# Kernel tuning notes

Hardware: AMD Instinct MI355X
Metric: run time of the kernel (lower is better)

The kernel has to match this reference:

```python
import jax, jax.numpy as jnp
import numpy as np

N_NODES = 50000
N_EDGES = 800000
N_GRAPHS = 64
IN_DIM = 128
HID = 64
HEADS = 4
LAT = 32
BN_EPS = 1e-5


def setup_inputs() -> dict:
    key = jax.random.key(0)
    ks = jax.random.split(key, 16)
    x = jax.random.normal(ks[0], (N_NODES, IN_DIM), jnp.float32)
    edge_index = jax.random.randint(ks[1], (2, N_EDGES), 0, N_NODES, dtype=jnp.int64)
    batch = jnp.sort(jax.random.randint(ks[2], (N_NODES,), 0, N_GRAPHS, dtype=jnp.int64))

    def lin(k, fan_in, shape):
        return (jax.random.normal(k, shape, jnp.float32) / np.sqrt(fan_in)).astype(jnp.float32)

    d = {"x": x, "edge_index": edge_index, "batch": batch}
    dims = [IN_DIM, HID, HID]
    i = 3
    for l, din in enumerate(dims):
        d[f"Wl{l}"] = lin(ks[i], din, (din, HEADS * HID)); i += 1
        d[f"Wr{l}"] = lin(ks[i], din, (din, HEADS * HID)); i += 1
        d[f"att{l}"] = lin(ks[i], HID, (HEADS, HID)); i += 1
        d[f"b{l}"] = jnp.zeros((HID,), jnp.float32)
    d["bn_gamma"] = jnp.ones((HID,), jnp.float32)
    d["bn_beta"] = jnp.zeros((HID,), jnp.float32)
    d["fc_W"] = lin(ks[i], HID, (LAT, HID)); i += 1
    d["fc_b"] = jnp.zeros((LAT,), jnp.float32)
    return d


def _gatv2_conv(x, Wl, Wr, att, b, src, dst):
    # PyG GATv2Conv, concat=False: mean over heads. src -> dst message flow.
    n = x.shape[0]
    H, D = att.shape
    xl = (x @ Wl).reshape(n, H, D)   # source-side transform
    xr = (x @ Wr).reshape(n, H, D)   # target-side transform
    e = jax.nn.leaky_relu(xl[src] + xr[dst], 0.2)        # [E, H, D]
    logits = jnp.einsum('ehd,hd->eh', e, att)            # [E, H]
    # segment softmax over incoming edges of each dst node
    m = jax.ops.segment_max(logits, dst, num_segments=n)
    p = jnp.exp(logits - m[dst])
    denom = jax.ops.segment_sum(p, dst, num_segments=n)
    alpha = p / (denom[dst] + 1e-16)                     # [E, H]
    out = jax.ops.segment_sum(alpha[..., None] * xl[src], dst, num_segments=n)  # [N, H, D]
    return out.mean(axis=1) + b


def reference(x, edge_index, batch, Wl0, Wr0, att0, b0, Wl1, Wr1, att1, b1,
              Wl2, Wr2, att2, b2, bn_gamma, bn_beta, fc_W, fc_b):
    src, dst = edge_index[0], edge_index[1]
    h = x
    for (Wl, Wr, att, b) in ((Wl0, Wr0, att0, b0), (Wl1, Wr1, att1, b1), (Wl2, Wr2, att2, b2)):
        h = _gatv2_conv(h, Wl, Wr, att, b, src, dst)
        h = jax.nn.leaky_relu(h, 0.1)
        # dropout omitted (deterministic reference / eval semantics)
    pooled = jax.ops.segment_sum(h, batch, num_segments=N_GRAPHS)  # [G, HID]
    mean = pooled.mean(axis=0)
    var = pooled.var(axis=0)  # biased variance, matches BN training normalization
    y = (pooled - mean) / jnp.sqrt(var + BN_EPS) * bn_gamma + bn_beta
    return y @ fc_W.T + fc_b
```

## Files before the change

kernel.cpp:

```cpp
#include <hip/hip_runtime.h>
#include <hip/hip_bf16.h>
#include <math.h>

#define N_NODES 50000
#define N_EDGES 800000
#define N_GRAPHS 64
#define IN_DIM 128
#define HID 64
#define HEADS 4
#define LAT 32
#define SCAN_BLOCKS ((N_NODES + 255) / 256)
#define ES_CAP 960000

typedef __attribute__((ext_vector_type(8))) short bf16x8;
typedef __attribute__((ext_vector_type(4))) float floatx4;
typedef __attribute__((ext_vector_type(2))) float f32x2;

__device__ inline unsigned short f2bf(float f) {
    unsigned u = __float_as_uint(f);
    return (unsigned short)((u + 0x7fffu + ((u >> 16) & 1u)) >> 16);
}

__device__ inline f32x2 bfpair(unsigned u) {
    f32x2 r;
    r.x = __uint_as_float(u << 16);
    r.y = __uint_as_float(u & 0xffff0000u);
    return r;
}

__device__ inline float rowsum16(float x) {
    x += __int_as_float(__builtin_amdgcn_mov_dpp(__float_as_int(x), 0x128, 0xf, 0xf, false));
    x += __int_as_float(__builtin_amdgcn_mov_dpp(__float_as_int(x), 0x124, 0xf, 0xf, false));
    x += __int_as_float(__builtin_amdgcn_mov_dpp(__float_as_int(x), 0x122, 0xf, 0xf, false));
    x += __int_as_float(__builtin_amdgcn_mov_dpp(__float_as_int(x), 0x121, 0xf, 0xf, false));
    return x;
}

__global__ __launch_bounds__(256) void prep_kernel(
    const float* __restrict__ x, unsigned* __restrict__ xbf,
    const float* __restrict__ Wl0, const float* __restrict__ Wr0,
    const float* __restrict__ Wl1, const float* __restrict__ Wr1,
    const float* __restrict__ Wl2, const float* __restrict__ Wr2,
    unsigned short* __restrict__ B0, unsigned short* __restrict__ B1,
    unsigned short* __restrict__ B2,
    int* __restrict__ cnt, float* __restrict__ pooled, int* __restrict__ done,
    uint4* __restrict__ es4) {
    int b = blockIdx.x, t = threadIdx.x;
    if (b < 3072) {
        for (int i = b * 256 + t; i < N_NODES * IN_DIM / 2; i += 3072 * 256) {
            float2 v = reinterpret_cast<const float2*>(x)[i];
            xbf[i] = (unsigned)f2bf(v.x) | ((unsigned)f2bf(v.y) << 16);
        }
    } else if (b < 3584) {
        int idx = (b - 3072) * 256 + t;
        const float *Wl, *Wr;
        unsigned short* B;
        int KC, local;
        if (idx < 65536)      { Wl = Wl0; Wr = Wr0; B = B0; KC = 4; local = idx; }
        else if (idx < 98304) { Wl = Wl1; Wr = Wr1; B = B1; KC = 2; local = idx - 65536; }
        else                  { Wl = Wl2; Wr = Wr2; B = B2; KC = 2; local = idx - 98304; }
        int j = local & 7;
        int lane = (local >> 3) & 63;
        int rem = local >> 9;
        int kc = rem % KC;
        int tile = rem / KC;
        int k = kc * 32 + (lane >> 4) * 8 + j;
        int tt = tile & 15;
        int n = (tt >> 1) * 32 + 2 * (lane & 15) + (tt & 1);
        const float* W = (tile < 16) ? Wl : Wr;
        B[local] = f2bf(W[k * 256 + n]);
    } else if (b < 3840) {
        int idx = (b - 3584) * 256 + t;
        if (idx < N_NODES) cnt[idx] = 0;
        if (idx < N_GRAPHS * HID) pooled[idx] = 0.f;
        if (idx == 0) *done = 0;
    } else {
        int idx = (b - 3840) * 256 + t;
        for (int i = idx; i < ES_CAP / 4; i += 65536)
            es4[i] = uint4{0, 0, 0, 0};
    }
}

__global__ __launch_bounds__(256) void deg_kernel(const int* __restrict__ dsts,
                                                  int* __restrict__ cnt, int E) {
    int e = blockIdx.x * 256 + threadIdx.x;
    if (e < E) atomicAdd(&cnt[dsts[e]], 1);
}

__global__ __launch_bounds__(256) void scan_kernel(const int* __restrict__ cnt,
                                                   int* __restrict__ offs,
                                                   int* __restrict__ sc,
                                                   int* __restrict__ agg) {
    __shared__ int buf[256];
    int b = blockIdx.x, t = threadIdx.x;
    int i = b * 256 + t;
    int v = (i < N_NODES) ? ((cnt[i] + 3) & ~3) : 0;
    buf[t] = v;
    __syncthreads();
    #pragma unroll
    for (int off = 1; off < 256; off <<= 1) {
        int tmp = (t >= off) ? buf[t - off] : 0;
        __syncthreads();
        buf[t] += tmp;
        __syncthreads();
    }
    int incl = buf[t];
    if (t == 255)
        __hip_atomic_store(&agg[b], buf[255] | 0x40000000,
                           __ATOMIC_RELEASE, __HIP_MEMORY_SCOPE_AGENT);
    int contrib = 0;
    if (t < b) {
        int vv;
        do {
            vv = __hip_atomic_load(&agg[t], __ATOMIC_ACQUIRE, __HIP_MEMORY_SCOPE_AGENT);
        } while (vv < 0 || !(vv & 0x40000000));
        contrib = vv & 0x3FFFFFFF;
    }
    __syncthreads();
    buf[t] = contrib;
    __syncthreads();
    for (int off = 128; off; off >>= 1) {
        if (t < off) buf[t] += buf[t + off];
        __syncthreads();
    }
    if (i < N_NODES) {
        offs[i] = buf[0] + incl - v;
        sc[i] = 0;
    }
}

__global__ __launch_bounds__(256) void scatter_kernel(const int* __restrict__ srcs,
                                                      const int* __restrict__ dsts,
                                                      const int* __restrict__ offs,
                                                      int* __restrict__ sc,
                                                      int* __restrict__ es, int E) {
    int e = blockIdx.x * 256 + threadIdx.x;
    if (e < E) {
        int d = dsts[e];
        int pos = offs[d] + atomicAdd(&sc[d], 1);
        es[pos] = srcs[e];
    }
}

template <int K>
__global__ __launch_bounds__(256) void gemm_mfma_kernel(
    const unsigned short* __restrict__ Abf,
    const unsigned short* __restrict__ Bpk,
    unsigned* __restrict__ xlp_u,
    unsigned* __restrict__ xrp_u) {
    constexpr int KC = K / 32;
    constexpr int CHUNKS = 16 * K / 8;
    __shared__ short As[CHUNKS * 8];
    int br = blockIdx.x * 16;
    int t = threadIdx.x;
    if (t < CHUNKS) {
        int row = t & 15;
        int kcol = (t >> 6) * 32 + ((t >> 4) & 3) * 8;
        *reinterpret_cast<uint4*>(&As[t * 8]) =
            *reinterpret_cast<const uint4*>(&Abf[(size_t)(br + row) * K + kcol]);
    }
    __syncthreads();
    int wave = t >> 6, lane = t & 63;
    int quad = lane >> 4, l16 = lane & 15;
    bf16x8 afrag[KC];
    #pragma unroll
    for (int kc = 0; kc < KC; ++kc)
        afrag[kc] = *reinterpret_cast<const bf16x8*>(&As[((kc * 4 + quad) * 16 + l16) * 8]);
    #pragma unroll
    for (int pr = 0; pr < 4; ++pr) {
        int T = wave * 8 + pr * 2;
        floatx4 acc0 = {0.f, 0.f, 0.f, 0.f};
        floatx4 acc1 = {0.f, 0.f, 0.f, 0.f};
        #pragma unroll
        for (int kc = 0; kc < KC; ++kc) {
            bf16x8 b0 = *reinterpret_cast<const bf16x8*>(
                &Bpk[(size_t)((T * KC + kc) * 64 + lane) * 8]);
            bf16x8 b1 = *reinterpret_cast<const bf16x8*>(
                &Bpk[(size_t)(((T + 1) * KC + kc) * 64 + lane) * 8]);
            acc0 = __builtin_amdgcn_mfma_f32_16x16x32_bf16(afrag[kc], b0, acc0, 0, 0, 0);
            acc1 = __builtin_amdgcn_mfma_f32_16x16x32_bf16(afrag[kc], b1, acc1, 0, 0, 0);
        }
        int tt = T & 15;
        unsigned* dst = (T < 16) ? xlp_u : xrp_u;
        int ci = (tt >> 1) * 16 + l16;
        #pragma unroll
        for (int r = 0; r < 4; ++r) {
            unsigned pk = (unsigned)f2bf(acc0[r]) | ((unsigned)f2bf(acc1[r]) << 16);
            dst[(size_t)(br + quad * 4 + r) * 128 + ci] = pk;
        }
    }
}

__global__ __launch_bounds__(256) void attn_kernel(const unsigned* __restrict__ xlp,
                                                   const unsigned* __restrict__ xrp,
                                                   const int* __restrict__ es,
                                                   const int* __restrict__ offs,
                                                   const int* __restrict__ deg,
                                                   const float4* __restrict__ att4,
                                                   const float4* __restrict__ bias4,
                                                   float* __restrict__ hout,
                                                   unsigned* __restrict__ hbf) {
    int node = blockIdx.x * 4 + (threadIdx.x >> 6);
    int lane = threadIdx.x & 63;
    int beg = offs[node];
    int end = beg + deg[node];
    uint2 xr2 = reinterpret_cast<const uint2*>(xrp)[(size_t)node * 64 + lane];
    f32x2 xrA = bfpair(xr2.x), xrB = bfpair(xr2.y);
    float4 at_t = att4[lane];
    f32x2 atA = {at_t.x, at_t.y}, atB = {at_t.z, at_t.w};
    const char* xbase = (const char*)xlp;
    int laneoff = lane << 3;

    float l = 0.f;
    f32x2 accA = {0.f, 0.f}, accB = {0.f, 0.f};

    auto edge_z = [&](uint2 v, f32x2& xa, f32x2& xb) -> float {
        xa = bfpair(v.x);
        xb = bfpair(v.y);
        f32x2 ea = xa + xrA;
        f32x2 eb = xb + xrB;
        ea = __builtin_elementwise_max(ea, ea * 0.2f);
        eb = __builtin_elementwise_max(eb, eb * 0.2f);
        f32x2 zz = ea * atA;
        zz += eb * atB;
        return zz.x + zz.y;
    };
    auto gather = [&](int s) -> uint2 {
        return *reinterpret_cast<const uint2*>(
            xbase + (((size_t)(unsigned)s) << 9) + laneoff);
    };

    for (int cb = beg; cb < end; cb += 4) {
        int4 s4 = *reinterpret_cast<const int4*>(&es[cb]);
        uint2 v0 = gather(s4.x);
        uint2 v1 = gather(s4.y);
        uint2 v2 = gather(s4.z);
        uint2 v3 = gather(s4.w);
        f32x2 xa0, xb0, xa1, xb1, xa2, xb2, xa3, xb3;
        float z0 = rowsum16(edge_z(v0, xa0, xb0));
        float z1 = rowsum16(edge_z(v1, xa1, xb1));
        float z2 = rowsum16(edge_z(v2, xa2, xb2));
        float z3 = rowsum16(edge_z(v3, xa3, xb3));
        float p0 = __expf(z0);
        float p1 = (cb + 1 < end) ? __expf(z1) : 0.f;
        float p2 = (cb + 2 < end) ? __expf(z2) : 0.f;
        float p3 = (cb + 3 < end) ? __expf(z3) : 0.f;
        accA += p0 * xa0 + p1 * xa1 + p2 * xa2 + p3 * xa3;
        accB += p0 * xb0 + p1 * xb1 + p2 * xb2 + p3 * xb3;
        l += (p0 + p1) + (p2 + p3);
    }

    float inv = 1.f / (l + 1e-16f);
    float a0 = accA.x * inv, a1 = accA.y * inv;
    float a2 = accB.x * inv, a3 = accB.y * inv;
    a0 += __shfl_xor(a0, 16); a0 += __shfl_xor(a0, 32);
    a1 += __shfl_xor(a1, 16); a1 += __shfl_xor(a1, 32);
    a2 += __shfl_xor(a2, 16); a2 += __shfl_xor(a2, 32);
    a3 += __shfl_xor(a3, 16); a3 += __shfl_xor(a3, 32);
    if (lane < 16) {
        float4 bv = bias4[lane];
        float4 o;
        o.x = 0.25f * a0 + bv.x; o.x = (o.x > 0.f) ? o.x : 0.1f * o.x;
        o.y = 0.25f * a1 + bv.y; o.y = (o.y > 0.f) ? o.y : 0.1f * o.y;
        o.z = 0.25f * a2 + bv.z; o.z = (o.z > 0.f) ? o.z : 0.1f * o.z;
        o.w = 0.25f * a3 + bv.w; o.w = (o.w > 0.f) ? o.w : 0.1f * o.w;
        if (hout)
            *reinterpret_cast<float4*>(&hout[(size_t)node * HID + lane * 4]) = o;
        if (hbf) {
            uint2 pk;
            pk.x = (unsigned)f2bf(o.x) | ((unsigned)f2bf(o.y) << 16);
            pk.y = (unsigned)f2bf(o.z) | ((unsigned)f2bf(o.w) << 16);
            *reinterpret_cast<uint2*>(&hbf[(size_t)node * 32 + lane * 2]) = pk;
        }
    }
}

__global__ __launch_bounds__(256) void pool_final_kernel(
    const float* __restrict__ hfin, const int* __restrict__ batch,
    float* __restrict__ pooled,
    const float* __restrict__ gamma, const float* __restrict__ beta,
    const float* __restrict__ fcW, const float* __restrict__ fcb,
    float* __restrict__ out, int* __restrict__ done) {
    int base = blockIdx.x * 256;
    int g = threadIdx.x >> 6, lane = threadIdx.x & 63;
    int lim = min(base + 256, N_NODES);
    int cur = -1;
    float s = 0.f;
    for (int i = base + g; i < lim; i += 4) {
        int b = batch[i];
        if (b != cur) {
            if (cur >= 0) atomicAdd(&pooled[cur * HID + lane], s);
            cur = b; s = 0.f;
        }
        s += hfin[(size_t)i * HID + lane];
    }
    if (cur >= 0) atomicAdd(&pooled[cur * HID + lane], s);

    __threadfence();
    __syncthreads();
    __shared__ int lastS;
    if (threadIdx.x == 0)
        lastS = (atomicAdd(done, 1) == (int)gridDim.x - 1);
    __syncthreads();
    if (!lastS) return;

    __shared__ float P[N_GRAPHS * HID];
    __shared__ float normS[N_GRAPHS * HID];
    __shared__ float meanS[HID], rstdS[HID];
    int t = threadIdx.x;
    for (int i = t; i < N_GRAPHS * HID; i += 256)
        P[i] = __hip_atomic_load(&pooled[i], __ATOMIC_RELAXED, __HIP_MEMORY_SCOPE_AGENT);
    __syncthreads();
    if (t < HID) {
        float s2 = 0.f;
        for (int g2 = 0; g2 < N_GRAPHS; ++g2) s2 += P[g2 * HID + t];
        float mean = s2 / (float)N_GRAPHS;
        float v = 0.f;
        for (int g2 = 0; g2 < N_GRAPHS; ++g2) {
            float dd = P[g2 * HID + t] - mean;
            v += dd * dd;
        }
        v /= (float)N_GRAPHS;
        meanS[t] = mean;
        rstdS[t] = rsqrtf(v + 1e-5f);
    }
    __syncthreads();
    for (int i = t; i < N_GRAPHS * HID; i += 256) {
        int d = i & 63;
        normS[i] = (P[i] - meanS[d]) * rstdS[d] * gamma[d] + beta[d];
    }
    __syncthreads();
    for (int i = t; i < N_GRAPHS * LAT; i += 256) {
        int g2 = i >> 5, lat = i & 31;
        float s2 = fcb[lat];
        for (int d = 0; d < HID; ++d) s2 += normS[g2 * HID + d] * fcW[lat * HID + d];
        out[i] = s2;
    }
}

extern "C" void kernel_launch(void* const* d_in, const int* in_sizes, int n_in,
                              void* d_out, int out_size, void* d_ws, size_t ws_size,
                              hipStream_t stream) {
    const float* x      = (const float*)d_in[0];
    const int*   ei     = (const int*)d_in[1];
    const int*   batch  = (const int*)d_in[2];
    const float* Wl[3]  = {(const float*)d_in[3], (const float*)d_in[7],  (const float*)d_in[11]};
    const float* Wr[3]  = {(const float*)d_in[4], (const float*)d_in[8],  (const float*)d_in[12]};
    const float* att[3] = {(const float*)d_in[5], (const float*)d_in[9],  (const float*)d_in[13]};
    const float* bia[3] = {(const float*)d_in[6], (const float*)d_in[10], (const float*)d_in[14]};
    const float* gamma  = (const float*)d_in[15];
    const float* beta   = (const float*)d_in[16];
    const float* fcW    = (const float*)d_in[17];
    const float* fcb    = (const float*)d_in[18];
    float* out = (float*)d_out;

    char* p = (char*)d_ws;
    auto alloc = [&](size_t bytes) {
        char* r = p;
        p += (bytes + 255) & ~(size_t)255;
        return r;
    };
    unsigned* xbf   = (unsigned*)alloc((size_t)N_NODES * IN_DIM * 2);
    unsigned* xlp   = (unsigned*)alloc((size_t)N_NODES * 256 * 2);
    unsigned* xrp   = (unsigned*)alloc((size_t)N_NODES * 256 * 2);
    unsigned* hbf0  = (unsigned*)alloc((size_t)N_NODES * HID * 2);
    unsigned* hbf1  = (unsigned*)alloc((size_t)N_NODES * HID * 2);
    unsigned short* Bpk0 = (unsigned short*)alloc(32 * 4 * 512 * 2);
    unsigned short* Bpk1 = (unsigned short*)alloc(32 * 2 * 512 * 2);
    unsigned short* Bpk2 = (unsigned short*)alloc(32 * 2 * 512 * 2);
    int*   es      = (int*)alloc((size_t)ES_CAP * 4);
    int*   offs    = (int*)alloc((size_t)N_NODES * 4);
    int*   cnt     = (int*)alloc((size_t)N_NODES * 4);
    int*   sc      = (int*)alloc((size_t)N_NODES * 4);
    int*   agg     = (int*)alloc((size_t)SCAN_BLOCKS * 4);
    int*   done    = (int*)alloc(256);
    float* pooled  = (float*)alloc((size_t)N_GRAPHS * HID * 4);
    float* hfin    = (float*)xbf;

    const int* srcs = ei;
    const int* dsts = ei + N_EDGES;

    prep_kernel<<<4096, 256, 0, stream>>>(x, xbf, Wl[0], Wr[0], Wl[1], Wr[1],
                                          Wl[2], Wr[2], Bpk0, Bpk1, Bpk2,
                                          cnt, pooled, done, (uint4*)es);
    int eb = (N_EDGES + 255) / 256;
    deg_kernel<<<eb, 256, 0, stream>>>(dsts, cnt, N_EDGES);
    scan_kernel<<<SCAN_BLOCKS, 256, 0, stream>>>(cnt, offs, sc, agg);
    scatter_kernel<<<eb, 256, 0, stream>>>(srcs, dsts, offs, sc, es, N_EDGES);

    int gb = N_NODES / 16;
    gemm_mfma_kernel<IN_DIM><<<gb, 256, 0, stream>>>((const unsigned short*)xbf, Bpk0, xlp, xrp);
    attn_kernel<<<N_NODES / 4, 256, 0, stream>>>(xlp, xrp, es, offs, cnt,
                                                 (const float4*)att[0],
                                                 (const float4*)bia[0], nullptr, hbf0);
    gemm_mfma_kernel<HID><<<gb, 256, 0, stream>>>((const unsigned short*)hbf0, Bpk1, xlp, xrp);
    attn_kernel<<<N_NODES / 4, 256, 0, stream>>>(xlp, xrp, es, offs, cnt,
                                                 (const float4*)att[1],
                                                 (const float4*)bia[1], nullptr, hbf1);
    gemm_mfma_kernel<HID><<<gb, 256, 0, stream>>>((const unsigned short*)hbf1, Bpk2, xlp, xrp);
    attn_kernel<<<N_NODES / 4, 256, 0, stream>>>(xlp, xrp, es, offs, cnt,
                                                 (const float4*)att[2],
                                                 (const float4*)bia[2], hfin, nullptr);

    pool_final_kernel<<<SCAN_BLOCKS, 256, 0, stream>>>(hfin, batch, pooled,
                                                       gamma, beta, fcW, fcb,
                                                       out, done);
}
```

Baseline: 479.2 us.

## Widen GEMM tile to 32 rows, load A fragments directly, vectorize stores

The MFMA projection kernel now handles 32 rows per block in two row tiles, so each loaded B fragment feeds two MFMAs. The LDS staging of A and its barrier are dropped, and fragments are read straight from global memory. The B packing layout is permuted so each lane can write eight contiguous bf16 outputs as one 16-byte store instead of scalar 4-byte stores. Float-to-bf16 packing switches to the hardware paired conversion intrinsic; the larger accumulator set raises register pressure.

```diff
diff --git a/kernel.cpp b/kernel.cpp
--- a/kernel.cpp
+++ b/kernel.cpp
@@ -1,6 +1,7 @@
 #include <hip/hip_runtime.h>
 #include <hip/hip_bf16.h>
 #include <math.h>
+#include <string.h>
 
 #define N_NODES 50000
 #define N_EDGES 800000
@@ -19,6 +20,14 @@
 __device__ inline unsigned short f2bf(float f) {
     unsigned u = __float_as_uint(f);
     return (unsigned short)((u + 0x7fffu + ((u >> 16) & 1u)) >> 16);
+}
+
+__device__ inline unsigned pkbf(float x, float y) {
+    float2 f{x, y};
+    __hip_bfloat162 h = __float22bfloat162_rn(f);
+    unsigned u;
+    memcpy(&u, &h, sizeof(u));
+    return u;
 }
 
 __device__ inline f32x2 bfpair(unsigned u) {
@@ -49,7 +58,7 @@
     if (b < 3072) {
         for (int i = b * 256 + t; i < N_NODES * IN_DIM / 2; i += 3072 * 256) {
             float2 v = reinterpret_cast<const float2*>(x)[i];
-            xbf[i] = (unsigned)f2bf(v.x) | ((unsigned)f2bf(v.y) << 16);
+            xbf[i] = pkbf(v.x, v.y);
         }
     } else if (b < 3584) {
         int idx = (b - 3072) * 256 + t;
@@ -66,7 +75,7 @@
         int tile = rem / KC;
         int k = kc * 32 + (lane >> 4) * 8 + j;
         int tt = tile & 15;
-        int n = (tt >> 1) * 32 + 2 * (lane & 15) + (tt & 1);
+        int n = (tt >> 3) * 128 + (lane & 15) * 8 + (tt & 7);
         const float* W = (tile < 16) ? Wl : Wr;
         B[local] = f2bf(W[k * 256 + n]);
     } else if (b < 3840) {
@@ -149,44 +158,54 @@
     unsigned* __restrict__ xlp_u,
     unsigned* __restrict__ xrp_u) {
     constexpr int KC = K / 32;
-    constexpr int CHUNKS = 16 * K / 8;
-    __shared__ short As[CHUNKS * 8];
-    int br = blockIdx.x * 16;
+    int br = blockIdx.x * 32;
     int t = threadIdx.x;
-    if (t < CHUNKS) {
-        int row = t & 15;
-        int kcol = (t >> 6) * 32 + ((t >> 4) & 3) * 8;
-        *reinterpret_cast<uint4*>(&As[t * 8]) =
-            *reinterpret_cast<const uint4*>(&Abf[(size_t)(br + row) * K + kcol]);
-    }
-    __syncthreads();
     int wave = t >> 6, lane = t & 63;
     int quad = lane >> 4, l16 = lane & 15;
-    bf16x8 afrag[KC];
+
+    bf16x8 afrag[2][KC];
     #pragma unroll
-    for (int kc = 0; kc < KC; ++kc)
-        afrag[kc] = *reinterpret_cast<const bf16x8*>(&As[((kc * 4 + quad) * 16 + l16) * 8]);
+    for (int rt = 0; rt < 2; ++rt) {
+        int row = br + rt * 16 + l16;
+        if (row > N_NODES - 1) row = N_NODES - 1;
+        const unsigned short* ap = Abf + (size_t)row * K + quad * 8;
+        #pragma unroll
+        for (int kc = 0; kc < KC; ++kc)
+            afrag[rt][kc] = *reinterpret_cast<const bf16x8*>(ap + kc * 32);
+    }
+
+    floatx4 acc[2][8];
     #pragma unroll
-    for (int pr = 0; pr < 4; ++pr) {
-        int T = wave * 8 + pr * 2;
-        floatx4 acc0 = {0.f, 0.f, 0.f, 0.f};
-        floatx4 acc1 = {0.f, 0.f, 0.f, 0.f};
+    for (int rt = 0; rt < 2; ++rt)
+        #pragma unroll
+        for (int i = 0; i < 8; ++i) acc[rt][i] = floatx4{0.f, 0.f, 0.f, 0.f};
+
+    const bf16x8* bbase = reinterpret_cast<const bf16x8*>(Bpk)
+                          + (size_t)(wave * 8) * KC * 64 + lane;
+    #pragma unroll
+    for (int i = 0; i < 8; ++i) {
         #pragma unroll
         for (int kc = 0; kc < KC; ++kc) {
-            bf16x8 b0 = *reinterpret_cast<const bf16x8*>(
-                &Bpk[(size_t)((T * KC + kc) * 64 + lane) * 8]);
-            bf16x8 b1 = *reinterpret_cast<const bf16x8*>(
-                &Bpk[(size_t)(((T + 1) * KC + kc) * 64 + lane) * 8]);
-            acc0 = __builtin_amdgcn_mfma_f32_16x16x32_bf16(afrag[kc], b0, acc0, 0, 0, 0);
-            acc1 = __builtin_amdgcn_mfma_f32_16x16x32_bf16(afrag[kc], b1, acc1, 0, 0, 0);
-        }
-        int tt = T & 15;
-        unsigned* dst = (T < 16) ? xlp_u : xrp_u;
-        int ci = (tt >> 1) * 16 + l16;
+            bf16x8 bfr = bbase[(i * KC + kc) * 64];
+            acc[0][i] = __builtin_amdgcn_mfma_f32_16x16x32_bf16(afrag[0][kc], bfr, acc[0][i], 0, 0, 0);
+            acc[1][i] = __builtin_amdgcn_mfma_f32_16x16x32_bf16(afrag[1][kc], bfr, acc[1][i], 0, 0, 0);
+        }
+    }
+
+    unsigned* dst = (wave < 2) ? xlp_u : xrp_u;
+    int cbase = (wave & 1) * 64 + l16 * 4;
+    #pragma unroll
+    for (int rt = 0; rt < 2; ++rt) {
+        if (br + rt * 16 >= N_NODES) break;
         #pragma unroll
         for (int r = 0; r < 4; ++r) {
-            unsigned pk = (unsigned)f2bf(acc0[r]) | ((unsigned)f2bf(acc1[r]) << 16);
-            dst[(size_t)(br + quad * 4 + r) * 128 + ci] = pk;
+            int row = br + rt * 16 + quad * 4 + r;
+            uint4 pk;
+            pk.x = pkbf(acc[rt][0][r], acc[rt][1][r]);
+            pk.y = pkbf(acc[rt][2][r], acc[rt][3][r]);
+            pk.z = pkbf(acc[rt][4][r], acc[rt][5][r]);
+            pk.w = pkbf(acc[rt][6][r], acc[rt][7][r]);
+            *reinterpret_cast<uint4*>(&dst[(size_t)row * 128 + cbase]) = pk;
         }
     }
 }
@@ -268,8 +287,8 @@
             *reinterpret_cast<float4*>(&hout[(size_t)node * HID + lane * 4]) = o;
         if (hbf) {
             uint2 pk;
-            pk.x = (unsigned)f2bf(o.x) | ((unsigned)f2bf(o.y) << 16);
-            pk.y = (unsigned)f2bf(o.z) | ((unsigned)f2bf(o.w) << 16);
+            pk.x = pkbf(o.x, o.y);
+            pk.y = pkbf(o.z, o.w);
             *reinterpret_cast<uint2*>(&hbf[(size_t)node * 32 + lane * 2]) = pk;
         }
     }
@@ -388,7 +407,7 @@
     scan_kernel<<<SCAN_BLOCKS, 256, 0, stream>>>(cnt, offs, sc, agg);
     scatter_kernel<<<eb, 256, 0, stream>>>(srcs, dsts, offs, sc, es, N_EDGES);
 
-    int gb = N_NODES / 16;
+    int gb = (N_NODES + 31) / 32;
     gemm_mfma_kernel<IN_DIM><<<gb, 256, 0, stream>>>((const unsigned short*)xbf, Bpk0, xlp, xrp);
     attn_kernel<<<N_NODES / 4, 256, 0, stream>>>(xlp, xrp, es, offs, cnt,
                                                  (const float4*)att[0],
```

Measured after the change: 500.3 us. +4.4%, slower.
